# Performance work log

Hardware: AMD Instinct MI355X
Metric: run time of the kernel (lower is better)

## Reference

```python
import jax, jax.numpy as jnp
import numpy as np

N_NODES = 100000
N_EDGES = 3200000


def gcn_conv(x, edge_index, W, b, n_nodes):
    # PyG GCNConv default: add self-loops, symmetric degree normalization,
    # linear transform, scatter-add aggregation at target nodes, add bias.
    src = jnp.concatenate([edge_index[0], jnp.arange(n_nodes, dtype=edge_index.dtype)])
    dst = jnp.concatenate([edge_index[1], jnp.arange(n_nodes, dtype=edge_index.dtype)])
    deg = jax.ops.segment_sum(jnp.ones_like(dst, dtype=x.dtype), dst, num_segments=n_nodes)
    dinv = jnp.where(deg > 0, jax.lax.rsqrt(jnp.maximum(deg, 1e-12)), 0.0)
    norm = dinv[src] * dinv[dst]            # [E+N]
    h = x @ W                               # [N, F_out]
    msg = h[src] * norm[:, None]            # gather + scale
    out = jax.ops.segment_sum(msg, dst, num_segments=n_nodes)
    return out + b


def setup_inputs() -> dict:
    key = jax.random.key(0)
    k1, k2, k3, k4 = jax.random.split(key, 4)
    x = jax.random.normal(k1, (N_NODES, 2), dtype=jnp.float32)
    edge_index = jax.random.randint(k2, (2, N_EDGES), 0, N_NODES, dtype=jnp.int64)
    # Glorot-ish init for weights, zero bias (PyG default zeros bias).
    W1 = jax.random.normal(k3, (2, 16), dtype=jnp.float32) * (1.0 / np.sqrt(2.0))
    b1 = jnp.zeros((16,), dtype=jnp.float32)
    W2 = jax.random.normal(k4, (16, 2), dtype=jnp.float32) * (1.0 / np.sqrt(16.0))
    b2 = jnp.zeros((2,), dtype=jnp.float32)
    return {"x": x, "edge_index": edge_index, "W1": W1, "b1": b1, "W2": W2, "b2": b2}


def reference(x, edge_index, W1, b1, W2, b2):
    n = x.shape[0]
    h = gcn_conv(x, edge_index, W1, b1, n)
    h = jax.nn.relu(h)
    h = gcn_conv(h, edge_index, W2, b2, n)
    return jax.nn.log_softmax(h, axis=1)
```

## Files before the change

kernel.cpp:

```cpp
#include <hip/hip_runtime.h>
#include <math.h>


#define BLK 256
#define NTILE 512
#define EPTMAX 6400
#define MAXB 512


__global__ void k_hist(const int* __restrict__ dst, int* __restrict__ table,
                       int e, int ept, int nbkt) {
    __shared__ int h[MAXB];
    int tile = blockIdx.x;
    for (int i = threadIdx.x; i < MAXB; i += BLK) h[i] = 0;
    __syncthreads();
    int lo = tile * ept;
    int hi = min(lo + ept, e);
    for (int i = lo + 4 * threadIdx.x; i < hi; i += 4 * BLK) {
        int4 d4 = *(const int4*)(dst + i);
        atomicAdd(&h[d4.x >> 8], 1);
        atomicAdd(&h[d4.y >> 8], 1);
        atomicAdd(&h[d4.z >> 8], 1);
        atomicAdd(&h[d4.w >> 8], 1);
    }
    __syncthreads();
    for (int i = threadIdx.x; i < nbkt; i += BLK)
        table[tile * nbkt + i] = h[i];
}

__global__ void k_scan_col(int* __restrict__ table, int* __restrict__ tot, int nbkt) {
    __shared__ int wsum[NTILE / 64];
    int b = blockIdx.x;
    int t = threadIdx.x;
    int v = table[t * nbkt + b];
    int x = v;
    int lane = t & 63;
#pragma unroll
    for (int ofs = 1; ofs < 64; ofs <<= 1) {
        int y = __shfl_up(x, ofs, 64);
        if (lane >= ofs) x += y;
    }
    if (lane == 63) wsum[t >> 6] = x;
    __syncthreads();
    if (t < NTILE / 64) {
        int s = wsum[t];
        int w = s;
#pragma unroll
        for (int ofs = 1; ofs < NTILE / 64; ofs <<= 1) {
            int y = __shfl_up(w, ofs, 64);
            if (t >= ofs) w += y;
        }
        wsum[t] = w - s;
    }
    __syncthreads();
    int incl = x + wsum[t >> 6];
    table[t * nbkt + b] = incl - v;
    if (t == NTILE - 1) tot[b] = incl;
}

__global__ void k_scan_tot(const int* __restrict__ tot, int* __restrict__ bkt_off, int nbkt) {
    __shared__ int wsum[MAXB / 64];
    int t = threadIdx.x;
    int v = (t < nbkt) ? tot[t] : 0;
    int x = v;
    int lane = t & 63;
#pragma unroll
    for (int ofs = 1; ofs < 64; ofs <<= 1) {
        int y = __shfl_up(x, ofs, 64);
        if (lane >= ofs) x += y;
    }
    if (lane == 63) wsum[t >> 6] = x;
    __syncthreads();
    if (t < MAXB / 64) {
        int s = wsum[t];
        int w = s;
#pragma unroll
        for (int ofs = 1; ofs < MAXB / 64; ofs <<= 1) {
            int y = __shfl_up(w, ofs, 64);
            if (t >= ofs) w += y;
        }
        wsum[t] = w - s;
    }
    __syncthreads();
    int incl = x + wsum[t >> 6];
    if (t < nbkt) bkt_off[t] = incl - v;
    if (t == nbkt - 1) bkt_off[nbkt] = incl;
}

__global__ void k_scatter(const int* __restrict__ src, const int* __restrict__ dst,
                          const int* __restrict__ table, const int* __restrict__ tot,
                          const int* __restrict__ bkt_off, unsigned* __restrict__ sorted,
                          int e, int ept, int nbkt) {
    __shared__ int cur[MAXB];
    __shared__ int base2[MAXB];
    __shared__ unsigned stage[EPTMAX];
    __shared__ unsigned short stage_b[EPTMAX];
    __shared__ int wpart[BLK / 64];
    int tile = blockIdx.x;
    int t = threadIdx.x;
    int lo = tile * ept;
    int hi = min(lo + ept, e);
    int total = hi - lo;

    int b0 = 2 * t, b1 = 2 * t + 1;
    int c0 = 0, c1 = 0, g0 = 0, g1 = 0;
    if (b0 < nbkt) {
        int base = table[tile * nbkt + b0];
        int next = (tile < NTILE - 1) ? table[(tile + 1) * nbkt + b0] : tot[b0];
        c0 = next - base;
        g0 = bkt_off[b0] + base;
    }
    if (b1 < nbkt) {
        int base = table[tile * nbkt + b1];
        int next = (tile < NTILE - 1) ? table[(tile + 1) * nbkt + b1] : tot[b1];
        c1 = next - base;
        g1 = bkt_off[b1] + base;
    }
    int p = c0 + c1;
    int x = p;
    int lane = t & 63;
#pragma unroll
    for (int ofs = 1; ofs < 64; ofs <<= 1) {
        int y = __shfl_up(x, ofs, 64);
        if (lane >= ofs) x += y;
    }
    if (lane == 63) wpart[t >> 6] = x;
    __syncthreads();
    if (t < BLK / 64) {
        int s = wpart[t];
        int w = s;
#pragma unroll
        for (int ofs = 1; ofs < BLK / 64; ofs <<= 1) {
            int y = __shfl_up(w, ofs, 64);
            if (t >= ofs) w += y;
        }
        wpart[t] = w - s;
    }
    __syncthreads();
    int E = x + wpart[t >> 6] - p;
    cur[b0] = E;
    cur[b1] = E + c0;
    if (b0 < nbkt) base2[b0] = g0 - E;
    if (b1 < nbkt) base2[b1] = g1 - (E + c0);
    __syncthreads();

    for (int i = lo + 4 * t; i < hi; i += 4 * BLK) {
        int4 s4 = *(const int4*)(src + i);
        int4 d4 = *(const int4*)(dst + i);
        int b, pos;
        b = d4.x >> 8; pos = atomicAdd(&cur[b], 1);
        stage[pos] = (unsigned)s4.x | ((unsigned)(d4.x & 255) << 17); stage_b[pos] = (unsigned short)b;
        b = d4.y >> 8; pos = atomicAdd(&cur[b], 1);
        stage[pos] = (unsigned)s4.y | ((unsigned)(d4.y & 255) << 17); stage_b[pos] = (unsigned short)b;
        b = d4.z >> 8; pos = atomicAdd(&cur[b], 1);
        stage[pos] = (unsigned)s4.z | ((unsigned)(d4.z & 255) << 17); stage_b[pos] = (unsigned short)b;
        b = d4.w >> 8; pos = atomicAdd(&cur[b], 1);
        stage[pos] = (unsigned)s4.w | ((unsigned)(d4.w & 255) << 17); stage_b[pos] = (unsigned short)b;
    }
    __syncthreads();
    for (int j = t; j < total; j += BLK) {
        int b = stage_b[j];
        sorted[base2[b] + j] = stage[j];
    }
}

__global__ __launch_bounds__(1024) void k_bsort(
        const unsigned* __restrict__ sorted, const int* __restrict__ bkt_off,
        const float* __restrict__ x, float* __restrict__ dinv,
        float* __restrict__ xp, unsigned* __restrict__ nsorted,
        int* __restrict__ nodeoff, int n) {
    __shared__ int cnt[256];
    __shared__ int cur[256];
    __shared__ int wsum[16];
    int b = blockIdx.x, t = threadIdx.x;
    if (t < 256) cnt[t] = 0;
    __syncthreads();
    int lo = bkt_off[b], hi = bkt_off[b + 1];
    int la = lo & ~3;
    for (int i = la + 4 * t; i < hi; i += 4 * 1024) {
        uint4 r = *(const uint4*)(sorted + i);
        if (i >= lo && i + 4 <= hi) {
            atomicAdd(&cnt[r.x >> 17], 1);
            atomicAdd(&cnt[r.y >> 17], 1);
            atomicAdd(&cnt[r.z >> 17], 1);
            atomicAdd(&cnt[r.w >> 17], 1);
        } else {
            if (i + 0 >= lo && i + 0 < hi) atomicAdd(&cnt[r.x >> 17], 1);
            if (i + 1 >= lo && i + 1 < hi) atomicAdd(&cnt[r.y >> 17], 1);
            if (i + 2 >= lo && i + 2 < hi) atomicAdd(&cnt[r.z >> 17], 1);
            if (i + 3 >= lo && i + 3 < hi) atomicAdd(&cnt[r.w >> 17], 1);
        }
    }
    __syncthreads();
    int c = (t < 256) ? cnt[t] : 0;
    int node = (b << 8) + t;
    if (t < 256 && node < n) {
        float d = rsqrtf((float)c + 1.0f);
        dinv[node] = d;
        float2 xv = ((const float2*)x)[node];
        ((float2*)xp)[node] = make_float2(d * xv.x, d * xv.y);
    }
    int xsc = c;
    int lane = t & 63;
#pragma unroll
    for (int ofs = 1; ofs < 64; ofs <<= 1) {
        int y = __shfl_up(xsc, ofs, 64);
        if (lane >= ofs) xsc += y;
    }
    if (lane == 63) wsum[t >> 6] = xsc;
    __syncthreads();
    if (t < 4) {
        int s = wsum[t];
        int w = s;
#pragma unroll
        for (int ofs = 1; ofs < 4; ofs <<= 1) {
            int y = __shfl_up(w, ofs, 64);
            if (t >= ofs) w += y;
        }
        wsum[t] = w - s;
    }
    __syncthreads();
    if (t < 256) {
        int excl = xsc + wsum[t >> 6] - c;
        cur[t] = excl;
        nodeoff[(b << 8) + t] = lo + excl;
    }
    __syncthreads();
    for (int i = la + 4 * t; i < hi; i += 4 * 1024) {
        uint4 r = *(const uint4*)(sorted + i);
        if (i >= lo && i + 4 <= hi) {
            int p0 = atomicAdd(&cur[r.x >> 17], 1); nsorted[lo + p0] = r.x & 0x1FFFFu;
            int p1 = atomicAdd(&cur[r.y >> 17], 1); nsorted[lo + p1] = r.y & 0x1FFFFu;
            int p2 = atomicAdd(&cur[r.z >> 17], 1); nsorted[lo + p2] = r.z & 0x1FFFFu;
            int p3 = atomicAdd(&cur[r.w >> 17], 1); nsorted[lo + p3] = r.w & 0x1FFFFu;
        } else {
            if (i + 0 >= lo && i + 0 < hi) { int p0 = atomicAdd(&cur[r.x >> 17], 1); nsorted[lo + p0] = r.x & 0x1FFFFu; }
            if (i + 1 >= lo && i + 1 < hi) { int p1 = atomicAdd(&cur[r.y >> 17], 1); nsorted[lo + p1] = r.y & 0x1FFFFu; }
            if (i + 2 >= lo && i + 2 < hi) { int p2 = atomicAdd(&cur[r.z >> 17], 1); nsorted[lo + p2] = r.z & 0x1FFFFu; }
            if (i + 3 >= lo && i + 3 < hi) { int p3 = atomicAdd(&cur[r.w >> 17], 1); nsorted[lo + p3] = r.w & 0x1FFFFu; }
        }
    }
}


__global__ void k_agg1(const unsigned* __restrict__ nsorted, const int* __restrict__ nodeoff,
                       const float* __restrict__ xp, const float* __restrict__ dinv,
                       const float* __restrict__ W1, const float* __restrict__ b1,
                       const float* __restrict__ W2, float* __restrict__ gp, int n) {
    int t = threadIdx.x;
    int nd = (blockIdx.x << 8) + (blockIdx.y << 6) + (t >> 2);
    int q = t & 3;
    if (nd >= n) return;
    int start = nodeoff[nd], end = nodeoff[nd + 1];
    const float2* xp2 = (const float2*)xp;
    float sx = 0.f, sy = 0.f;
    for (int p = (start & ~3) + 4 * q; p < end; p += 16) {
        uint4 r = *(const uint4*)(nsorted + p);
        if (p >= start && p + 4 <= end) {
            float2 f0 = xp2[r.x], f1 = xp2[r.y], f2 = xp2[r.z], f3 = xp2[r.w];
            sx += (f0.x + f1.x) + (f2.x + f3.x);
            sy += (f0.y + f1.y) + (f2.y + f3.y);
        } else {
            if (p + 0 >= start && p + 0 < end) { float2 f = xp2[r.x]; sx += f.x; sy += f.y; }
            if (p + 1 >= start && p + 1 < end) { float2 f = xp2[r.y]; sx += f.x; sy += f.y; }
            if (p + 2 >= start && p + 2 < end) { float2 f = xp2[r.z]; sx += f.x; sy += f.y; }
            if (p + 3 >= start && p + 3 < end) { float2 f = xp2[r.w]; sx += f.x; sy += f.y; }
        }
    }
    sx += __shfl_xor(sx, 1); sy += __shfl_xor(sy, 1);
    sx += __shfl_xor(sx, 2); sy += __shfl_xor(sy, 2);
    if (q == 0) {
        float d = dinv[nd];
        float2 xv = xp2[nd];
        float ax = d * (sx + xv.x), ay = d * (sy + xv.y);
        float g0 = 0.f, g1 = 0.f;
#pragma unroll
        for (int f = 0; f < 16; ++f) {
            float h = fmaf(ax, W1[f], fmaf(ay, W1[16 + f], b1[f]));
            h = fmaxf(h, 0.0f);
            g0 = fmaf(h, W2[2 * f + 0], g0);
            g1 = fmaf(h, W2[2 * f + 1], g1);
        }
        ((float2*)gp)[nd] = make_float2(d * g0, d * g1);
    }
}

__global__ void k_agg2(const unsigned* __restrict__ nsorted, const int* __restrict__ nodeoff,
                       const float* __restrict__ gp, const float* __restrict__ dinv,
                       const float* __restrict__ b2, float* __restrict__ out, int n) {
    int t = threadIdx.x;
    int nd = (blockIdx.x << 8) + (blockIdx.y << 6) + (t >> 2);
    int q = t & 3;
    if (nd >= n) return;
    int start = nodeoff[nd], end = nodeoff[nd + 1];
    const float2* gp2 = (const float2*)gp;
    float sx = 0.f, sy = 0.f;
    for (int p = (start & ~3) + 4 * q; p < end; p += 16) {
        uint4 r = *(const uint4*)(nsorted + p);
        if (p >= start && p + 4 <= end) {
            float2 f0 = gp2[r.x], f1 = gp2[r.y], f2 = gp2[r.z], f3 = gp2[r.w];
            sx += (f0.x + f1.x) + (f2.x + f3.x);
            sy += (f0.y + f1.y) + (f2.y + f3.y);
        } else {
            if (p + 0 >= start && p + 0 < end) { float2 f = gp2[r.x]; sx += f.x; sy += f.y; }
            if (p + 1 >= start && p + 1 < end) { float2 f = gp2[r.y]; sx += f.x; sy += f.y; }
            if (p + 2 >= start && p + 2 < end) { float2 f = gp2[r.z]; sx += f.x; sy += f.y; }
            if (p + 3 >= start && p + 3 < end) { float2 f = gp2[r.w]; sx += f.x; sy += f.y; }
        }
    }
    sx += __shfl_xor(sx, 1); sy += __shfl_xor(sy, 1);
    sx += __shfl_xor(sx, 2); sy += __shfl_xor(sy, 2);
    if (q == 0) {
        float d = dinv[nd];
        float2 gv = gp2[nd];
        float z0 = d * (sx + gv.x) + b2[0];
        float z1 = d * (sy + gv.y) + b2[1];
        float m = fmaxf(z0, z1);
        float lse = m + logf(expf(z0 - m) + expf(z1 - m));
        ((float2*)out)[nd] = make_float2(z0 - lse, z1 - lse);
    }
}

extern "C" void kernel_launch(void* const* d_in, const int* in_sizes, int n_in,
                              void* d_out, int out_size, void* d_ws, size_t ws_size,
                              hipStream_t stream) {
    const float* x  = (const float*)d_in[0];
    const int*   ei = (const int*)d_in[1];
    const float* W1 = (const float*)d_in[2];
    const float* b1 = (const float*)d_in[3];
    const float* W2 = (const float*)d_in[4];
    const float* b2 = (const float*)d_in[5];
    float* out = (float*)d_out;

    const int n = in_sizes[0] / 2;
    const int e = in_sizes[1] / 2;
    const int* src = ei;
    const int* dst = ei + e;

    const int nbkt = (n + 255) >> 8;
    int ept = (((e + NTILE - 1) / NTILE) + 3) & ~3;

    char* base = (char*)d_ws;
    size_t off = 0;
    auto take = [&](size_t bytes) { char* p = base + off; off += (bytes + 255) & ~(size_t)255; return p; };
    unsigned* sorted  = (unsigned*)take(((size_t)e + 8) * 4);
    int*      table   = (int*)take((size_t)NTILE * nbkt * 4);
    int*      tot     = (int*)take((size_t)MAXB * 4);
    int*      bkt_off = (int*)take((size_t)(MAXB + 1) * 4);
    unsigned* nsorted = (unsigned*)take(((size_t)e + 8) * 4);
    int*      nodeoff = (int*)take((size_t)(nbkt * 256 + 64) * 4);
    float*    dinv    = (float*)take((size_t)n * 4);
    float*    xp      = (float*)take((size_t)n * 8);
    float*    gp      = (float*)take((size_t)n * 8);

    dim3 gagg(nbkt, 4);

    k_hist    <<<NTILE, BLK, 0, stream>>>(dst, table, e, ept, nbkt);
    k_scan_col<<<nbkt, NTILE, 0, stream>>>(table, tot, nbkt);
    k_scan_tot<<<1, MAXB, 0, stream>>>(tot, bkt_off, nbkt);
    k_scatter <<<NTILE, BLK, 0, stream>>>(src, dst, table, tot, bkt_off, sorted, e, ept, nbkt);
    k_bsort   <<<nbkt, 1024, 0, stream>>>(sorted, bkt_off, x, dinv, xp, nsorted, nodeoff, n);
    k_agg1    <<<gagg, BLK, 0, stream>>>(nsorted, nodeoff, xp, dinv, W1, b1, W2, gp, n);
    k_agg2    <<<gagg, BLK, 0, stream>>>(nsorted, nodeoff, gp, dinv, b2, out, n);
}
```

Before: 158.1 us.

## Fuse layer-1 aggregation into bucket sort using shared-memory float atomics

Splits the bucket sort into a degree/offset kernel and a second pass. The second pass scatters source indices into node order and also accumulates the layer-1 gathered features per destination node with LDS float atomics, then applies the dense MLP to produce gp. This drops the separate k_agg1 pass and its re-read of nsorted, at the cost of re-reading the staged bucket data in the new kernel and adding heavy LDS atomic contention. Float atomics also make the summation order nondeterministic.

After: 171.8 us. 1.09x slower.

```diff
diff --git a/kernel.cpp b/kernel.cpp
--- a/kernel.cpp
+++ b/kernel.cpp
@@ -28,7 +28,8 @@
         table[tile * nbkt + i] = h[i];
 }
 
-__global__ void k_scan_col(int* __restrict__ table, int* __restrict__ tot, int nbkt) {
+__global__ __launch_bounds__(NTILE) void k_scan_col(
+        int* __restrict__ table, int* __restrict__ tot, int nbkt) {
     __shared__ int wsum[NTILE / 64];
     int b = blockIdx.x;
     int t = threadIdx.x;
@@ -164,13 +165,11 @@
     }
 }
 
-__global__ __launch_bounds__(1024) void k_bsort(
+__global__ __launch_bounds__(1024) void k_deg(
         const unsigned* __restrict__ sorted, const int* __restrict__ bkt_off,
         const float* __restrict__ x, float* __restrict__ dinv,
-        float* __restrict__ xp, unsigned* __restrict__ nsorted,
-        int* __restrict__ nodeoff, int n) {
+        float* __restrict__ xp, int* __restrict__ nodeoff, int n) {
     __shared__ int cnt[256];
-    __shared__ int cur[256];
     __shared__ int wsum[16];
     int b = blockIdx.x, t = threadIdx.x;
     if (t < 256) cnt[t] = 0;
@@ -220,59 +219,64 @@
         wsum[t] = w - s;
     }
     __syncthreads();
+    if (t < 256)
+        nodeoff[(b << 8) + t] = lo + xsc + wsum[t >> 6] - c;
+}
+
+__global__ __launch_bounds__(1024) void k_bsort2(
+        const unsigned* __restrict__ sorted, const int* __restrict__ bkt_off,
+        const int* __restrict__ nodeoff, const float* __restrict__ xp,
+        const float* __restrict__ dinv,
+        const float* __restrict__ W1, const float* __restrict__ b1,
+        const float* __restrict__ W2,
+        unsigned* __restrict__ nsorted, float* __restrict__ gp, int n) {
+    __shared__ int cur[256];
+    __shared__ float accx[256];
+    __shared__ float accy[256];
+    int b = blockIdx.x, t = threadIdx.x;
     if (t < 256) {
-        int excl = xsc + wsum[t >> 6] - c;
-        cur[t] = excl;
-        nodeoff[(b << 8) + t] = lo + excl;
-    }
-    __syncthreads();
+        cur[t] = nodeoff[(b << 8) + t];
+        accx[t] = 0.f;
+        accy[t] = 0.f;
+    }
+    __syncthreads();
+    int lo = bkt_off[b], hi = bkt_off[b + 1];
+    int la = lo & ~3;
+    const float2* xp2 = (const float2*)xp;
     for (int i = la + 4 * t; i < hi; i += 4 * 1024) {
         uint4 r = *(const uint4*)(sorted + i);
         if (i >= lo && i + 4 <= hi) {
-            int p0 = atomicAdd(&cur[r.x >> 17], 1); nsorted[lo + p0] = r.x & 0x1FFFFu;
-            int p1 = atomicAdd(&cur[r.y >> 17], 1); nsorted[lo + p1] = r.y & 0x1FFFFu;
-            int p2 = atomicAdd(&cur[r.z >> 17], 1); nsorted[lo + p2] = r.z & 0x1FFFFu;
-            int p3 = atomicAdd(&cur[r.w >> 17], 1); nsorted[lo + p3] = r.w & 0x1FFFFu;
+            int s0 = r.x & 0x1FFFFu, d0 = r.x >> 17;
+            int s1 = r.y & 0x1FFFFu, d1 = r.y >> 17;
+            int s2 = r.z & 0x1FFFFu, d2 = r.z >> 17;
+            int s3 = r.w & 0x1FFFFu, d3 = r.w >> 17;
+            float2 f0 = xp2[s0], f1 = xp2[s1], f2 = xp2[s2], f3 = xp2[s3];
+            int p0 = atomicAdd(&cur[d0], 1); nsorted[p0] = (unsigned)s0;
+            int p1 = atomicAdd(&cur[d1], 1); nsorted[p1] = (unsigned)s1;
+            int p2 = atomicAdd(&cur[d2], 1); nsorted[p2] = (unsigned)s2;
+            int p3 = atomicAdd(&cur[d3], 1); nsorted[p3] = (unsigned)s3;
+            atomicAdd(&accx[d0], f0.x); atomicAdd(&accy[d0], f0.y);
+            atomicAdd(&accx[d1], f1.x); atomicAdd(&accy[d1], f1.y);
+            atomicAdd(&accx[d2], f2.x); atomicAdd(&accy[d2], f2.y);
+            atomicAdd(&accx[d3], f3.x); atomicAdd(&accy[d3], f3.y);
         } else {
-            if (i + 0 >= lo && i + 0 < hi) { int p0 = atomicAdd(&cur[r.x >> 17], 1); nsorted[lo + p0] = r.x & 0x1FFFFu; }
-            if (i + 1 >= lo && i + 1 < hi) { int p1 = atomicAdd(&cur[r.y >> 17], 1); nsorted[lo + p1] = r.y & 0x1FFFFu; }
-            if (i + 2 >= lo && i + 2 < hi) { int p2 = atomicAdd(&cur[r.z >> 17], 1); nsorted[lo + p2] = r.z & 0x1FFFFu; }
-            if (i + 3 >= lo && i + 3 < hi) { int p3 = atomicAdd(&cur[r.w >> 17], 1); nsorted[lo + p3] = r.w & 0x1FFFFu; }
-        }
-    }
-}
-
-
-__global__ void k_agg1(const unsigned* __restrict__ nsorted, const int* __restrict__ nodeoff,
-                       const float* __restrict__ xp, const float* __restrict__ dinv,
-                       const float* __restrict__ W1, const float* __restrict__ b1,
-                       const float* __restrict__ W2, float* __restrict__ gp, int n) {
-    int t = threadIdx.x;
-    int nd = (blockIdx.x << 8) + (blockIdx.y << 6) + (t >> 2);
-    int q = t & 3;
-    if (nd >= n) return;
-    int start = nodeoff[nd], end = nodeoff[nd + 1];
-    const float2* xp2 = (const float2*)xp;
-    float sx = 0.f, sy = 0.f;
-    for (int p = (start & ~3) + 4 * q; p < end; p += 16) {
-        uint4 r = *(const uint4*)(nsorted + p);
-        if (p >= start && p + 4 <= end) {
-            float2 f0 = xp2[r.x], f1 = xp2[r.y], f2 = xp2[r.z], f3 = xp2[r.w];
-            sx += (f0.x + f1.x) + (f2.x + f3.x);
-            sy += (f0.y + f1.y) + (f2.y + f3.y);
-        } else {
-            if (p + 0 >= start && p + 0 < end) { float2 f = xp2[r.x]; sx += f.x; sy += f.y; }
-            if (p + 1 >= start && p + 1 < end) { float2 f = xp2[r.y]; sx += f.x; sy += f.y; }
-            if (p + 2 >= start && p + 2 < end) { float2 f = xp2[r.z]; sx += f.x; sy += f.y; }
-            if (p + 3 >= start && p + 3 < end) { float2 f = xp2[r.w]; sx += f.x; sy += f.y; }
-        }
-    }
-    sx += __shfl_xor(sx, 1); sy += __shfl_xor(sy, 1);
-    sx += __shfl_xor(sx, 2); sy += __shfl_xor(sy, 2);
-    if (q == 0) {
-        float d = dinv[nd];
-        float2 xv = xp2[nd];
-        float ax = d * (sx + xv.x), ay = d * (sy + xv.y);
+            unsigned rr[4] = {r.x, r.y, r.z, r.w};
+            for (int k = 0; k < 4; ++k) {
+                if (i + k >= lo && i + k < hi) {
+                    int s = rr[k] & 0x1FFFFu, d = rr[k] >> 17;
+                    float2 f = xp2[s];
+                    int p = atomicAdd(&cur[d], 1); nsorted[p] = (unsigned)s;
+                    atomicAdd(&accx[d], f.x); atomicAdd(&accy[d], f.y);
+                }
+            }
+        }
+    }
+    __syncthreads();
+    int node = (b << 8) + t;
+    if (t < 256 && node < n) {
+        float d = dinv[node];
+        float2 xv = xp2[node];
+        float ax = d * (accx[t] + xv.x), ay = d * (accy[t] + xv.y);
         float g0 = 0.f, g1 = 0.f;
 #pragma unroll
         for (int f = 0; f < 16; ++f) {
@@ -281,7 +285,7 @@
             g0 = fmaf(h, W2[2 * f + 0], g0);
             g1 = fmaf(h, W2[2 * f + 1], g1);
         }
-        ((float2*)gp)[nd] = make_float2(d * g0, d * g1);
+        ((float2*)gp)[node] = make_float2(d * g0, d * g1);
     }
 }
 
@@ -359,7 +363,7 @@
     k_scan_col<<<nbkt, NTILE, 0, stream>>>(table, tot, nbkt);
     k_scan_tot<<<1, MAXB, 0, stream>>>(tot, bkt_off, nbkt);
     k_scatter <<<NTILE, BLK, 0, stream>>>(src, dst, table, tot, bkt_off, sorted, e, ept, nbkt);
-    k_bsort   <<<nbkt, 1024, 0, stream>>>(sorted, bkt_off, x, dinv, xp, nsorted, nodeoff, n);
-    k_agg1    <<<gagg, BLK, 0, stream>>>(nsorted, nodeoff, xp, dinv, W1, b1, W2, gp, n);
+    k_deg     <<<nbkt, 1024, 0, stream>>>(sorted, bkt_off, x, dinv, xp, nodeoff, n);
+    k_bsort2  <<<nbkt, 1024, 0, stream>>>(sorted, bkt_off, nodeoff, xp, dinv, W1, b1, W2, nsorted, gp, n);
     k_agg2    <<<gagg, BLK, 0, stream>>>(nsorted, nodeoff, gp, dinv, b2, out, n);
 }
```
